# Kernel optimization log

Measured on AMD Instinct MI355X. Metric: run time of the kernel, lower is better.

The kernel has to match this reference:

```python
import jax, jax.numpy as jnp
import numpy as np

CAPACITY_FACTOR = 1.2


def setup_inputs() -> dict:
    key = jax.random.key(0)
    k1, k2, k3 = jax.random.split(key, 3)
    B, S, D, E = 8, 4096, 512, 16
    x = jax.random.normal(k1, (B, S, D), dtype=jnp.float32)
    switch_w = jax.random.normal(k2, (E, D), dtype=jnp.float32) * 0.02
    switch_b = jnp.zeros((E,), dtype=jnp.float32)
    expert_w = jax.random.normal(k3, (E, D, D), dtype=jnp.float32) * 0.02
    expert_b = jnp.zeros((E, D), dtype=jnp.float32)
    return {"x": x, "switch_w": switch_w, "switch_b": switch_b,
            "expert_w": expert_w, "expert_b": expert_b}


def reference(x, switch_w, switch_b, expert_w, expert_b):
    B, S, D = x.shape
    E = switch_w.shape[0]
    N = B * S
    xf = x.reshape(N, D)

    # Router: softmax over experts, top-1 route.
    logits = xf @ switch_w.T + switch_b            # [N, E]
    probs = jax.nn.softmax(logits, axis=-1)
    route_probs = jnp.max(probs, axis=-1)          # [N]
    routes = jnp.argmax(probs, axis=-1)            # [N] int

    # Position of each token within its expert's queue (token order).
    oh = jax.nn.one_hot(routes, E, dtype=jnp.int32)            # [N, E]
    pos = jnp.take_along_axis(jnp.cumsum(oh, axis=0), routes[:, None], axis=1)[:, 0] - 1  # [N]

    capacity = int(CAPACITY_FACTOR * N / E)        # static
    keep = pos < capacity                          # [N] bool; overflow tokens dropped

    # Dispatch: scatter kept tokens into [E, capacity, D] buffer.
    # Out-of-capacity positions are out-of-bounds and dropped by scatter semantics.
    buf = jnp.zeros((E, capacity, D), dtype=xf.dtype).at[routes, pos].set(xf)

    # Per-expert Linear (torch Linear: y = x @ W.T + b), as one grouped GEMM.
    y = jnp.einsum('ecd,efd->ecf', buf, expert_w) + expert_b[:, None, :]  # [E, C, D]

    # Combine: gather expert outputs back; dropped tokens pass through x.
    gathered = y[routes, jnp.minimum(pos, capacity - 1)]       # [N, D]
    out = jnp.where(keep[:, None], gathered, xf) * route_probs[:, None]
    return out.reshape(B, S, D)
```

## Files before the change

kernel.cpp:

```cpp
#include <hip/hip_runtime.h>
#include <math.h>

#define N_TOK 32768
#define DIM   512
#define NEXP  16
#define CAP   2457
#define CAPP  2464
#define NCHUNK 512

typedef __attribute__((ext_vector_type(8))) short   short8;
typedef __attribute__((ext_vector_type(4))) short   short4v;
typedef __attribute__((ext_vector_type(4))) float   floatx4;

__device__ __forceinline__ short f2bf(float f) {
  unsigned u = __builtin_bit_cast(unsigned, f);
  unsigned r = u + 0x7FFFu + ((u >> 16) & 1u);
  return (short)(r >> 16);
}

__global__ __launch_bounds__(256) void router_k(
    const float* __restrict__ x, const float* __restrict__ sw,
    const float* __restrict__ sb, int* __restrict__ route,
    float* __restrict__ prob, int* __restrict__ hist,
    short* __restrict__ x_bf) {
  __shared__ int lcnt[NEXP];
  int tid = threadIdx.x;
  if (tid < NEXP) lcnt[tid] = 0;
  __syncthreads();
  int wv = tid >> 6, lane = tid & 63;
  int base = blockIdx.x * 64 + wv * 16;

  float4 wA[NEXP], wB[NEXP];
#pragma unroll
  for (int e = 0; e < NEXP; ++e) {
    const float4* wr = (const float4*)(sw + e * DIM);
    wA[e] = wr[lane]; wB[e] = wr[lane + 64];
  }

  for (int i = 0; i < 16; ++i) {
    int t = base + i;
    const float4* xr = (const float4*)(x + (size_t)t * DIM);
    float4 xa = xr[lane], xb = xr[lane + 64];

    short4v sa, sbv;
    sa[0] = f2bf(xa.x); sa[1] = f2bf(xa.y); sa[2] = f2bf(xa.z); sa[3] = f2bf(xa.w);
    sbv[0] = f2bf(xb.x); sbv[1] = f2bf(xb.y); sbv[2] = f2bf(xb.z); sbv[3] = f2bf(xb.w);
    short4v* xo = (short4v*)(x_bf + (size_t)t * DIM);
    xo[lane] = sa; xo[lane + 64] = sbv;

    float p[NEXP];
#pragma unroll
    for (int e = 0; e < NEXP; ++e)
      p[e] = xa.x*wA[e].x + xa.y*wA[e].y + xa.z*wA[e].z + xa.w*wA[e].w
           + xb.x*wB[e].x + xb.y*wB[e].y + xb.z*wB[e].z + xb.w*wB[e].w;
#pragma unroll
    for (int m = 1; m < 64; m <<= 1) {
#pragma unroll
      for (int e = 0; e < NEXP; ++e) p[e] += __shfl_xor(p[e], m, 64);
    }
    if (lane == 0) {
      int arg = 0; float mx = p[0] + sb[0];
      float lg[NEXP];
      lg[0] = mx;
#pragma unroll
      for (int e = 1; e < NEXP; ++e) {
        lg[e] = p[e] + sb[e];
        if (lg[e] > mx) { mx = lg[e]; arg = e; }
      }
      float s = 0.f;
#pragma unroll
      for (int e = 0; e < NEXP; ++e) s += expf(lg[e] - mx);
      route[t] = arg;
      prob[t]  = 1.0f / s;
      atomicAdd(&lcnt[arg], 1);
    }
  }
  __syncthreads();
  if (tid < NEXP) hist[blockIdx.x * NEXP + tid] = lcnt[tid];
}

__global__ __launch_bounds__(256) void convw_k(
    const float* __restrict__ ew, short* __restrict__ w_bf) {
  int i = blockIdx.x * 256 + threadIdx.x;
  float4 f = ((const float4*)ew)[i];
  short4v s;
  s[0] = f2bf(f.x); s[1] = f2bf(f.y); s[2] = f2bf(f.z); s[3] = f2bf(f.w);
  ((short4v*)w_bf)[i] = s;
}

__global__ __launch_bounds__(256) void scan_k(
    const int* __restrict__ hist, int* __restrict__ offs,
    int* __restrict__ counts) {
  __shared__ int part[16][NEXP];
  __shared__ int base[16][NEXP];
  int e = threadIdx.x & 15, g = threadIdx.x >> 4;
  int s = 0;
  for (int b = g * 32; b < g * 32 + 32; ++b) s += hist[b * NEXP + e];
  part[g][e] = s;
  __syncthreads();
  if (g == 0) {
    int run = 0;
#pragma unroll
    for (int gg = 0; gg < 16; ++gg) { base[gg][e] = run; run += part[gg][e]; }
    counts[e] = run;
  }
  __syncthreads();
  int run = base[g][e];
  for (int b = g * 32; b < g * 32 + 32; ++b) {
    offs[b * NEXP + e] = run;
    run += hist[b * NEXP + e];
  }
}

__global__ __launch_bounds__(64) void pos_k(
    const int* __restrict__ route, const float* __restrict__ prob,
    const int* __restrict__ offs, const float* __restrict__ x,
    float* __restrict__ out, int* __restrict__ lists) {
  int tid = threadIdx.x;
  int t = blockIdx.x * 64 + tid;
  int r = route[t];
  unsigned long long lower = (1ull << tid) - 1ull;
  int rank = 0;
#pragma unroll
  for (int e = 0; e < NEXP; ++e) {
    unsigned long long m = __ballot(r == e);
    if (r == e) rank = __popcll(m & lower);
  }
  int pos = offs[blockIdx.x * NEXP + r] + rank;
  if (pos < CAP) {
    lists[r * CAPP + pos] = t;
  } else {
    float p = prob[t];
    const float4* xr = (const float4*)(x + (size_t)t * DIM);
    float4* o = (float4*)(out + (size_t)t * DIM);
    for (int d = 0; d < DIM / 4; ++d) {
      float4 v = xr[d];
      v.x *= p; v.y *= p; v.z *= p; v.w *= p;
      o[d] = v;
    }
  }
}

#define BM 128
#define BN 128
#define BKS 64

__global__ __launch_bounds__(256, 2) void gemm_k(
    const short* __restrict__ x_bf, const short* __restrict__ w_bf,
    const float* __restrict__ eb, const int* __restrict__ lists,
    const int* __restrict__ counts, const float* __restrict__ prob,
    float* __restrict__ out) {
  int e = blockIdx.z;
  int cnt = counts[e]; if (cnt > CAP) cnt = CAP;
  int row0 = blockIdx.y * BM;
  if (row0 >= cnt) return;
  int col0 = blockIdx.x * BN;

  __shared__ short A_s[BM * BKS];
  __shared__ short B_s[BN * BKS];
  __shared__ int rowtok[BM];

  int tid = threadIdx.x;
  if (tid < BM) {
    int gr = row0 + tid;
    rowtok[tid] = (gr < cnt) ? lists[e * CAPP + gr] : 0;
  }
  __syncthreads();

  int wv = tid >> 6, lane = tid & 63;
  int q = lane >> 4, l16 = lane & 15;
  int wrow = (wv >> 1) * 64, wcol = (wv & 1) * 64;

  int r_loc = lane >> 3, c = lane & 7;
  int g = c ^ r_loc;
  const short* ga[4]; const short* gb[4];
  short* la[4]; short* lb[4];
#pragma unroll
  for (int t4 = 0; t4 < 4; ++t4) {
    int row = wv * 32 + t4 * 8 + r_loc;
    ga[t4] = x_bf + (size_t)rowtok[row] * DIM + g * 8;
    gb[t4] = w_bf + (size_t)(e * DIM + col0 + row) * DIM + g * 8;
    la[t4] = &A_s[(wv * 32 + t4 * 8) * BKS];
    lb[t4] = &B_s[(wv * 32 + t4 * 8) * BKS];
  }

  floatx4 acc[4][4] = {};

  for (int k0 = 0; k0 < DIM; k0 += BKS) {
#pragma unroll
    for (int t4 = 0; t4 < 4; ++t4) {
      __builtin_amdgcn_global_load_lds(
          (const __attribute__((address_space(1))) void*)(ga[t4] + k0),
          (__attribute__((address_space(3))) void*)(la[t4]), 16, 0, 0);
      __builtin_amdgcn_global_load_lds(
          (const __attribute__((address_space(1))) void*)(gb[t4] + k0),
          (__attribute__((address_space(3))) void*)(lb[t4]), 16, 0, 0);
    }
    __syncthreads();
#pragma unroll
    for (int kk = 0; kk < 2; ++kk) {
      short8 af[4], bfv[4];
      int ckbase = kk * 4 + q;
#pragma unroll
      for (int sm = 0; sm < 4; ++sm) {
        int row = wrow + sm * 16 + l16;
        int ph = ckbase ^ (row & 7);
        af[sm] = *(const short8*)&A_s[row * BKS + ph * 8];
      }
#pragma unroll
      for (int sn = 0; sn < 4; ++sn) {
        int row = wcol + sn * 16 + l16;
        int ph = ckbase ^ (row & 7);
        bfv[sn] = *(const short8*)&B_s[row * BKS + ph * 8];
      }
#pragma unroll
      for (int sm = 0; sm < 4; ++sm)
#pragma unroll
        for (int sn = 0; sn < 4; ++sn)
          acc[sm][sn] = __builtin_amdgcn_mfma_f32_16x16x32_bf16(
              af[sm], bfv[sn], acc[sm][sn], 0, 0, 0);
    }
    __syncthreads();
  }

#pragma unroll
  for (int sm = 0; sm < 4; ++sm) {
    int tt[4]; float pp[4]; int vld[4];
#pragma unroll
    for (int rg = 0; rg < 4; ++rg) {
      int rr = wrow + sm * 16 + q * 4 + rg;
      int gr = row0 + rr;
      vld[rg] = (gr < cnt);
      tt[rg]  = rowtok[rr];
      pp[rg]  = vld[rg] ? prob[tt[rg]] : 0.f;
    }
#pragma unroll
    for (int sn = 0; sn < 4; ++sn) {
      int col = col0 + wcol + sn * 16 + l16;
      float bias = eb[e * DIM + col];
#pragma unroll
      for (int rg = 0; rg < 4; ++rg)
        if (vld[rg])
          out[(size_t)tt[rg] * DIM + col] = (acc[sm][sn][rg] + bias) * pp[rg];
    }
  }
}

extern "C" void kernel_launch(void* const* d_in, const int* in_sizes, int n_in,
                              void* d_out, int out_size, void* d_ws, size_t ws_size,
                              hipStream_t stream) {
  const float* x  = (const float*)d_in[0];
  const float* sw = (const float*)d_in[1];
  const float* sb = (const float*)d_in[2];
  const float* ew = (const float*)d_in[3];
  const float* eb = (const float*)d_in[4];
  float* out = (float*)d_out;

  char* ws = (char*)d_ws;
  int*   route  = (int*)(ws + 0);
  float* prob   = (float*)(ws + 131072);
  int*   hist   = (int*)(ws + 262144);
  int*   offs   = (int*)(ws + 294912);
  int*   counts = (int*)(ws + 327680);
  int*   lists  = (int*)(ws + 327744);
  short* x_bf   = (short*)(ws + (1 << 20));
  short* w_bf   = (short*)(ws + (1 << 20) + 33554432);

  hipLaunchKernelGGL(router_k, dim3(NCHUNK), dim3(256), 0, stream,
                     x, sw, sb, route, prob, hist, x_bf);
  hipLaunchKernelGGL(convw_k, dim3(NEXP * DIM * DIM / 4 / 256), dim3(256), 0, stream,
                     ew, w_bf);
  hipLaunchKernelGGL(scan_k, dim3(1), dim3(256), 0, stream, hist, offs, counts);
  hipLaunchKernelGGL(pos_k, dim3(NCHUNK), dim3(64), 0, stream,
                     route, prob, offs, x, out, lists);
  hipLaunchKernelGGL(gemm_k, dim3(4, 20, 16), dim3(256), 0, stream,
                     x_bf, w_bf, eb, lists, counts, prob, out);
}
```

Measured before the change: 218.8 us.

## Compute router logits with split-bf16 MFMA and fuse weight conversion into router

The router now computes token-by-expert logits with MFMA instructions, using a hi/lo bf16 split of both x and the switch weights so the result stays close to fp32 accuracy. This replaces per-lane FMAs and a 16-value shuffle reduction per token. The expert-weight fp32-to-bf16 conversion is folded into the router kernel, which removes one launch. The per-block histogram is now built with ballots instead of shared atomics. The risks are a small change in logit precision that could flip near-tied argmax routes, and extra per-block work from staging the switch weights in shared memory.

Result: faster. 184.7 us (-15.6%).

```diff
diff --git a/kernel.cpp b/kernel.cpp
--- a/kernel.cpp
+++ b/kernel.cpp
@@ -17,75 +17,106 @@
   unsigned r = u + 0x7FFFu + ((u >> 16) & 1u);
   return (short)(r >> 16);
 }
-
+__device__ __forceinline__ float bf2f(short h) {
+  return __builtin_bit_cast(float, ((unsigned)(unsigned short)h) << 16);
+}
+
+#define LGP 17
 __global__ __launch_bounds__(256) void router_k(
     const float* __restrict__ x, const float* __restrict__ sw,
-    const float* __restrict__ sb, int* __restrict__ route,
-    float* __restrict__ prob, int* __restrict__ hist,
-    short* __restrict__ x_bf) {
-  __shared__ int lcnt[NEXP];
+    const float* __restrict__ sb, const float* __restrict__ ew,
+    int* __restrict__ route, float* __restrict__ prob, int* __restrict__ hist,
+    short* __restrict__ x_bf, short* __restrict__ w_bf) {
+  __shared__ short swh[16][520];
+  __shared__ short swl[16][520];
+  __shared__ float lgt[64][LGP];
+  __shared__ float sbs[NEXP];
+
   int tid = threadIdx.x;
-  if (tid < NEXP) lcnt[tid] = 0;
-  __syncthreads();
-  int wv = tid >> 6, lane = tid & 63;
-  int base = blockIdx.x * 64 + wv * 16;
-
-  float4 wA[NEXP], wB[NEXP];
-#pragma unroll
-  for (int e = 0; e < NEXP; ++e) {
-    const float4* wr = (const float4*)(sw + e * DIM);
-    wA[e] = wr[lane]; wB[e] = wr[lane + 64];
-  }
-
-  for (int i = 0; i < 16; ++i) {
-    int t = base + i;
-    const float4* xr = (const float4*)(x + (size_t)t * DIM);
-    float4 xa = xr[lane], xb = xr[lane + 64];
-
-    short4v sa, sbv;
-    sa[0] = f2bf(xa.x); sa[1] = f2bf(xa.y); sa[2] = f2bf(xa.z); sa[3] = f2bf(xa.w);
-    sbv[0] = f2bf(xb.x); sbv[1] = f2bf(xb.y); sbv[2] = f2bf(xb.z); sbv[3] = f2bf(xb.w);
-    short4v* xo = (short4v*)(x_bf + (size_t)t * DIM);
-    xo[lane] = sa; xo[lane + 64] = sbv;
-
-    float p[NEXP];
-#pragma unroll
-    for (int e = 0; e < NEXP; ++e)
-      p[e] = xa.x*wA[e].x + xa.y*wA[e].y + xa.z*wA[e].z + xa.w*wA[e].w
-           + xb.x*wB[e].x + xb.y*wB[e].y + xb.z*wB[e].z + xb.w*wB[e].w;
-#pragma unroll
-    for (int m = 1; m < 64; m <<= 1) {
-#pragma unroll
-      for (int e = 0; e < NEXP; ++e) p[e] += __shfl_xor(p[e], m, 64);
-    }
-    if (lane == 0) {
-      int arg = 0; float mx = p[0] + sb[0];
-      float lg[NEXP];
-      lg[0] = mx;
-#pragma unroll
-      for (int e = 1; e < NEXP; ++e) {
-        lg[e] = p[e] + sb[e];
-        if (lg[e] > mx) { mx = lg[e]; arg = e; }
-      }
-      float s = 0.f;
-#pragma unroll
-      for (int e = 0; e < NEXP; ++e) s += expf(lg[e] - mx);
-      route[t] = arg;
-      prob[t]  = 1.0f / s;
-      atomicAdd(&lcnt[arg], 1);
-    }
-  }
-  __syncthreads();
-  if (tid < NEXP) hist[blockIdx.x * NEXP + tid] = lcnt[tid];
-}
-
-__global__ __launch_bounds__(256) void convw_k(
-    const float* __restrict__ ew, short* __restrict__ w_bf) {
-  int i = blockIdx.x * 256 + threadIdx.x;
-  float4 f = ((const float4*)ew)[i];
-  short4v s;
-  s[0] = f2bf(f.x); s[1] = f2bf(f.y); s[2] = f2bf(f.z); s[3] = f2bf(f.w);
-  ((short4v*)w_bf)[i] = s;
+
+  {
+    const float4* src = (const float4*)ew;
+    short4v* dst = (short4v*)w_bf;
+    int base = blockIdx.x * 2048 + tid;
+#pragma unroll
+    for (int i = 0; i < 8; ++i) {
+      float4 f = src[base + i * 256];
+      short4v s;
+      s[0] = f2bf(f.x); s[1] = f2bf(f.y); s[2] = f2bf(f.z); s[3] = f2bf(f.w);
+      dst[base + i * 256] = s;
+    }
+  }
+
+  {
+    int idx = tid;
+#pragma unroll
+    for (int i = 0; i < 8; ++i, idx += 256) {
+      int e = idx >> 7, k4 = idx & 127;
+      float4 f = ((const float4*)(sw + e * DIM))[k4];
+      short4v h, l;
+      h[0] = f2bf(f.x); h[1] = f2bf(f.y); h[2] = f2bf(f.z); h[3] = f2bf(f.w);
+      l[0] = f2bf(f.x - bf2f(h[0]));
+      l[1] = f2bf(f.y - bf2f(h[1]));
+      l[2] = f2bf(f.z - bf2f(h[2]));
+      l[3] = f2bf(f.w - bf2f(h[3]));
+      *(short4v*)&swh[e][k4 * 4] = h;
+      *(short4v*)&swl[e][k4 * 4] = l;
+    }
+  }
+  if (tid < NEXP) sbs[tid] = sb[tid];
+  __syncthreads();
+
+  int wv = tid >> 6, lane = tid & 63, q = lane >> 4, l16 = lane & 15;
+  int row = blockIdx.x * 64 + wv * 16 + l16;
+  const float* xr = x + (size_t)row * DIM;
+  short* xbr = x_bf + (size_t)row * DIM;
+
+  floatx4 acc = {};
+#pragma unroll 4
+  for (int kc = 0; kc < 16; ++kc) {
+    int k0 = kc * 32 + q * 8;
+    float4 f0 = *(const float4*)(xr + k0);
+    float4 f1 = *(const float4*)(xr + k0 + 4);
+    short8 hi, lo;
+    hi[0] = f2bf(f0.x); hi[1] = f2bf(f0.y); hi[2] = f2bf(f0.z); hi[3] = f2bf(f0.w);
+    hi[4] = f2bf(f1.x); hi[5] = f2bf(f1.y); hi[6] = f2bf(f1.z); hi[7] = f2bf(f1.w);
+    lo[0] = f2bf(f0.x - bf2f(hi[0])); lo[1] = f2bf(f0.y - bf2f(hi[1]));
+    lo[2] = f2bf(f0.z - bf2f(hi[2])); lo[3] = f2bf(f0.w - bf2f(hi[3]));
+    lo[4] = f2bf(f1.x - bf2f(hi[4])); lo[5] = f2bf(f1.y - bf2f(hi[5]));
+    lo[6] = f2bf(f1.z - bf2f(hi[6])); lo[7] = f2bf(f1.w - bf2f(hi[7]));
+    *(short8*)(xbr + k0) = hi;
+    short8 bh = *(const short8*)&swh[l16][k0];
+    short8 bl = *(const short8*)&swl[l16][k0];
+    acc = __builtin_amdgcn_mfma_f32_16x16x32_bf16(hi, bh, acc, 0, 0, 0);
+    acc = __builtin_amdgcn_mfma_f32_16x16x32_bf16(lo, bh, acc, 0, 0, 0);
+    acc = __builtin_amdgcn_mfma_f32_16x16x32_bf16(hi, bl, acc, 0, 0, 0);
+    acc = __builtin_amdgcn_mfma_f32_16x16x32_bf16(lo, bl, acc, 0, 0, 0);
+  }
+#pragma unroll
+  for (int r = 0; r < 4; ++r)
+    lgt[wv * 16 + q * 4 + r][l16] = acc[r];
+  __syncthreads();
+
+  if (tid < 64) {
+    int t = blockIdx.x * 64 + tid;
+    float lg[NEXP];
+#pragma unroll
+    for (int e = 0; e < NEXP; ++e) lg[e] = lgt[tid][e] + sbs[e];
+    int arg = 0; float mx = lg[0];
+#pragma unroll
+    for (int e = 1; e < NEXP; ++e)
+      if (lg[e] > mx) { mx = lg[e]; arg = e; }
+    float s = 0.f;
+#pragma unroll
+    for (int e = 0; e < NEXP; ++e) s += expf(lg[e] - mx);
+    route[t] = arg;
+    prob[t]  = 1.0f / s;
+#pragma unroll
+    for (int e = 0; e < NEXP; ++e) {
+      unsigned long long m = __ballot(arg == e);
+      if (tid == e) hist[blockIdx.x * NEXP + e] = __popcll(m);
+    }
+  }
 }
 
 __global__ __launch_bounds__(256) void scan_k(
@@ -267,9 +298,7 @@
   short* w_bf   = (short*)(ws + (1 << 20) + 33554432);
 
   hipLaunchKernelGGL(router_k, dim3(NCHUNK), dim3(256), 0, stream,
-                     x, sw, sb, route, prob, hist, x_bf);
-  hipLaunchKernelGGL(convw_k, dim3(NEXP * DIM * DIM / 4 / 256), dim3(256), 0, stream,
-                     ew, w_bf);
+                     x, sw, sb, ew, route, prob, hist, x_bf, w_bf);
   hipLaunchKernelGGL(scan_k, dim3(1), dim3(256), 0, stream, hist, offs, counts);
   hipLaunchKernelGGL(pos_k, dim3(NCHUNK), dim3(64), 0, stream,
                      route, prob, offs, x, out, lists);
```
